# Kernel optimization log

Measured on AMD Instinct MI355X. Metric: run time of the kernel, lower is better.

The kernel has to match this reference:

```python
import jax, jax.numpy as jnp
import numpy as np

N_NODES = 100000
N_EDGES = 1600000
NODE_DIM = 128
EDGE_DIM = 32
HIDDEN = 64
OUT = 64


def setup_inputs() -> dict:
    key = jax.random.key(0)
    ks = jax.random.split(key, 16)
    s = lambda d: 1.0 / np.sqrt(d)
    inp = {
        'node_features': jax.random.normal(ks[0], (N_NODES, NODE_DIM), dtype=jnp.float32),
        'edge_indices': jax.random.randint(ks[1], (2, N_EDGES), 0, N_NODES, dtype=jnp.int64),
        'edge_features': jax.random.normal(ks[2], (N_EDGES, EDGE_DIM), dtype=jnp.float32),
        # node_transform / edge_transform
        'wn': jax.random.uniform(ks[3], (NODE_DIM, HIDDEN), jnp.float32, -s(NODE_DIM), s(NODE_DIM)),
        'bn': jax.random.uniform(ks[4], (HIDDEN,), jnp.float32, -s(NODE_DIM), s(NODE_DIM)),
        'we': jax.random.uniform(ks[5], (EDGE_DIM, HIDDEN), jnp.float32, -s(EDGE_DIM), s(EDGE_DIM)),
        'be': jax.random.uniform(ks[6], (HIDDEN,), jnp.float32, -s(EDGE_DIM), s(EDGE_DIM)),
        # message_mlp: Linear(2H,H) -> ReLU -> Linear(H,OUT)
        'wm1': jax.random.uniform(ks[7], (2 * HIDDEN, HIDDEN), jnp.float32, -s(2 * HIDDEN), s(2 * HIDDEN)),
        'bm1': jax.random.uniform(ks[8], (HIDDEN,), jnp.float32, -s(2 * HIDDEN), s(2 * HIDDEN)),
        'wm2': jax.random.uniform(ks[9], (HIDDEN, OUT), jnp.float32, -s(HIDDEN), s(HIDDEN)),
        'bm2': jax.random.uniform(ks[10], (OUT,), jnp.float32, -s(HIDDEN), s(HIDDEN)),
        # update_mlp: Linear(NODE_DIM+OUT,H) -> ReLU -> Linear(H,OUT)
        'wu1': jax.random.uniform(ks[11], (NODE_DIM + OUT, HIDDEN), jnp.float32, -s(NODE_DIM + OUT), s(NODE_DIM + OUT)),
        'bu1': jax.random.uniform(ks[12], (HIDDEN,), jnp.float32, -s(NODE_DIM + OUT), s(NODE_DIM + OUT)),
        'wu2': jax.random.uniform(ks[13], (HIDDEN, OUT), jnp.float32, -s(HIDDEN), s(HIDDEN)),
        'bu2': jax.random.uniform(ks[14], (OUT,), jnp.float32, -s(HIDDEN), s(HIDDEN)),
    }
    return inp


def reference(node_features, edge_indices, edge_features, wn, bn, we, be,
              wm1, bm1, wm2, bm2, wu1, bu1, wu2, bu2):
    node_emb = node_features @ wn + bn              # [N, H]
    edge_emb = edge_features @ we + be              # [E, H]
    src, dst = edge_indices[0], edge_indices[1]
    messages = jnp.concatenate([node_emb[src], edge_emb], axis=-1)  # [E, 2H]
    messages = jax.nn.relu(messages @ wm1 + bm1) @ wm2 + bm2        # [E, OUT]
    aggregated = jax.ops.segment_sum(messages, dst, num_segments=node_emb.shape[0])  # [N, OUT]
    updated = jnp.concatenate([node_features, aggregated], axis=-1)  # [N, NODE_DIM+OUT]
    return jax.nn.relu(updated @ wu1 + bu1) @ wu2 + bu2              # [N, OUT]
```

## Files before the change

### kernel.cpp

```cpp
#include <hip/hip_runtime.h>

#define NN 100000
#define NE 1600000

typedef __attribute__((ext_vector_type(8))) short bf16x8;
typedef __attribute__((ext_vector_type(4))) float f32x4;

#define OFF_M    0
#define OFF_B    (OFF_M + 16384)
#define OFF_C    (OFF_B + 2048)
#define OFF_W2U  (OFF_C + 64)
#define OFF_D2   (OFF_W2U + 4096)
#define OFF_BFRG (OFF_D2 + 64)
#define OFF_MFRG (OFF_BFRG + 1024)
#define OFF_W2UF (OFF_MFRG + 8192)
#define OFF_WU2F (OFF_W2UF + 2048)
#define OFF_BSUM (OFF_WU2F + 2048)
#define OFF_BOFF (OFF_BSUM + 128)
#define OFF_PRA  (OFF_BOFF + 128)
#define OFF_PRAH (OFF_PRA + NN * 64)
#define OFF_PRU  (OFF_PRAH + NN * 32)
#define OFF_H    (OFF_PRU + NN * 64)
#define OFF_HIST (OFF_H + NN * 64)
#define OFF_CUR  (OFF_HIST + NN)
#define OFF_STRT (OFF_CUR + NN)
#define OFF_HS   (OFF_STRT + NN + 4)
#define WS_UNITS (OFF_HS + NE * 32)

__device__ __forceinline__ unsigned bfr(float x) {
  unsigned u = __float_as_uint(x);
  return (u + 0x7fffu + ((u >> 16) & 1u)) >> 16;
}
__device__ __forceinline__ float bf2f(unsigned short h) {
  return __uint_as_float(((unsigned)h) << 16);
}
__device__ __forceinline__ unsigned addrelu1(unsigned qa, unsigned pb) {
  float lo = __uint_as_float((qa & 0xffffu) << 16) +
             __uint_as_float((pb & 0xffffu) << 16);
  float hi = __uint_as_float(qa & 0xffff0000u) +
             __uint_as_float(pb & 0xffff0000u);
  lo = fmaxf(lo, 0.f);
  hi = fmaxf(hi, 0.f);
  return bfr(lo) | (bfr(hi) << 16);
}
__device__ __forceinline__ uint4 addrelu4(uint4 q, uint4 p) {
  return make_uint4(addrelu1(q.x, p.x), addrelu1(q.y, p.y),
                    addrelu1(q.z, p.z), addrelu1(q.w, p.w));
}

__global__ __launch_bounds__(256) void k_fold(
    const float* __restrict__ wn, const float* __restrict__ bn,
    const float* __restrict__ we, const float* __restrict__ be,
    const float* __restrict__ wm1, const float* __restrict__ bm1,
    const float* __restrict__ wm2, const float* __restrict__ bm2,
    const float* __restrict__ wu1, const float* __restrict__ wu2,
    float* __restrict__ M, float* __restrict__ B, float* __restrict__ c,
    float* __restrict__ W2U, float* __restrict__ d2,
    uint4* __restrict__ Bfrag, uint4* __restrict__ Mfrag,
    uint4* __restrict__ W2Uf, uint4* __restrict__ wu2f) {
  int t = blockIdx.x * 256 + threadIdx.x;
  if (t < 16384) {
    int k = t >> 7, j = t & 127;
    float acc;
    if (j < 64) {
      acc = 0.f;
      for (int h = 0; h < 64; ++h) acc += wn[k * 64 + h] * wm1[h * 64 + j];
    } else {
      acc = wu1[k * 64 + (j - 64)];
    }
    M[t] = acc;
  } else if (t < 16384 + 2048) {
    int u = t - 16384;
    int k = u >> 6, j = u & 63;
    float acc = 0.f;
    for (int h = 0; h < 64; ++h) acc += we[k * 64 + h] * wm1[(64 + h) * 64 + j];
    B[u] = acc;
  } else if (t < 16384 + 2048 + 64) {
    int j = t - (16384 + 2048);
    float acc = bm1[j];
    for (int h = 0; h < 64; ++h)
      acc += bn[h] * wm1[h * 64 + j] + be[h] * wm1[(64 + h) * 64 + j];
    c[j] = acc;
  } else if (t < 16384 + 2048 + 64 + 4096) {
    int u = t - (16384 + 2048 + 64);
    int k = u >> 6, j = u & 63;
    float acc = 0.f;
    for (int h = 0; h < 64; ++h) acc += wm2[k * 64 + h] * wu1[(128 + h) * 64 + j];
    W2U[u] = acc;
  } else if (t < 16384 + 2048 + 64 + 4096 + 64) {
    int j = t - (16384 + 2048 + 64 + 4096);
    float acc = 0.f;
    for (int h = 0; h < 64; ++h) acc += bm2[h] * wu1[(128 + h) * 64 + j];
    d2[j] = acc;
  } else if (t < 16384 + 2048 + 64 + 4096 + 64 + 256) {
    int u = t - (16384 + 2048 + 64 + 4096 + 64);
    int jb = u >> 6, l = u & 63;
    int g = l >> 4, n = l & 15;
    unsigned s[8];
#pragma unroll
    for (int i = 0; i < 8; ++i) {
      int k = g * 8 + i;
      int j = jb * 16 + n;
      float acc = 0.f;
      for (int h = 0; h < 64; ++h)
        acc += we[k * 64 + h] * wm1[(64 + h) * 64 + j];
      s[i] = bfr(acc);
    }
    Bfrag[jb * 64 + l] = make_uint4(s[0] | (s[1] << 16), s[2] | (s[3] << 16),
                                    s[4] | (s[5] << 16), s[6] | (s[7] << 16));
  } else if (t < 16384 + 2048 + 64 + 4096 + 64 + 256 + 2048) {
    int u = t - (16384 + 2048 + 64 + 4096 + 64 + 256);
    int jb = u >> 8, kb = (u >> 6) & 3, l = u & 63;
    int g = l >> 4, n = l & 15;
    int j = jb * 16 + n;
    unsigned s[8];
#pragma unroll
    for (int i = 0; i < 8; ++i) {
      int k = kb * 32 + g * 8 + i;
      float acc;
      if (j < 64) {
        acc = 0.f;
        for (int h = 0; h < 64; ++h) acc += wn[k * 64 + h] * wm1[h * 64 + j];
      } else {
        acc = wu1[k * 64 + (j - 64)];
      }
      s[i] = bfr(acc);
    }
    Mfrag[(jb * 4 + kb) * 64 + l] =
        make_uint4(s[0] | (s[1] << 16), s[2] | (s[3] << 16),
                   s[4] | (s[5] << 16), s[6] | (s[7] << 16));
  } else if (t < 16384 + 2048 + 64 + 4096 + 64 + 256 + 2048 + 512) {
    int u = t - (16384 + 2048 + 64 + 4096 + 64 + 256 + 2048);
    int jk = u >> 6, l = u & 63;
    int jb = jk >> 1, kb = jk & 1;
    int g = l >> 4, n = l & 15;
    int j = jb * 16 + n;
    unsigned s[8];
#pragma unroll
    for (int i = 0; i < 8; ++i) {
      int k = kb * 32 + g * 8 + i;
      float acc = 0.f;
      for (int h = 0; h < 64; ++h)
        acc += wm2[k * 64 + h] * wu1[(128 + h) * 64 + j];
      s[i] = bfr(acc);
    }
    W2Uf[jk * 64 + l] = make_uint4(s[0] | (s[1] << 16), s[2] | (s[3] << 16),
                                   s[4] | (s[5] << 16), s[6] | (s[7] << 16));
  } else if (t < 16384 + 2048 + 64 + 4096 + 64 + 256 + 2048 + 512 + 512) {
    int u = t - (16384 + 2048 + 64 + 4096 + 64 + 256 + 2048 + 512);
    int jk = u >> 6, l = u & 63;
    int jb = jk >> 1, kb = jk & 1;
    int g = l >> 4, n = l & 15;
    unsigned s[8];
#pragma unroll
    for (int i = 0; i < 8; ++i)
      s[i] = bfr(wu2[(size_t)(kb * 32 + g * 8 + i) * 64 + jb * 16 + n]);
    wu2f[jk * 64 + l] = make_uint4(s[0] | (s[1] << 16), s[2] | (s[3] << 16),
                                   s[4] | (s[5] << 16), s[6] | (s[7] << 16));
  }
}

__global__ __launch_bounds__(256) void k_node2(
    const float* __restrict__ nf, const uint4* __restrict__ Mfrag,
    float* __restrict__ PRA, float* __restrict__ PRU) {
  int wib = threadIdx.x >> 6;
  int lane = threadIdx.x & 63;
  int tile = blockIdx.x * 4 + wib;
  if (tile >= NN / 16) return;
  int m = lane & 15, g = lane >> 4;
  int node = tile * 16 + m;

  bf16x8 a[4];
#pragma unroll
  for (int kb = 0; kb < 4; ++kb) {
    const float* __restrict__ rp = &nf[(size_t)node * 128 + kb * 32 + g * 8];
    float4 f0 = *(const float4*)rp;
    float4 f1 = *(const float4*)(rp + 4);
    bf16x8 v;
    v[0] = (short)bfr(f0.x); v[1] = (short)bfr(f0.y);
    v[2] = (short)bfr(f0.z); v[3] = (short)bfr(f0.w);
    v[4] = (short)bfr(f1.x); v[5] = (short)bfr(f1.y);
    v[6] = (short)bfr(f1.z); v[7] = (short)bfr(f1.w);
    a[kb] = v;
  }

  const bf16x8* __restrict__ mfp = (const bf16x8*)Mfrag;
#pragma unroll
  for (int jb = 0; jb < 8; ++jb) {
    f32x4 acc = {0.f, 0.f, 0.f, 0.f};
    acc = __builtin_amdgcn_mfma_f32_16x16x32_bf16(a[0], mfp[(jb * 4 + 0) * 64 + lane], acc, 0, 0, 0);
    acc = __builtin_amdgcn_mfma_f32_16x16x32_bf16(a[1], mfp[(jb * 4 + 1) * 64 + lane], acc, 0, 0, 0);
    acc = __builtin_amdgcn_mfma_f32_16x16x32_bf16(a[2], mfp[(jb * 4 + 2) * 64 + lane], acc, 0, 0, 0);
    acc = __builtin_amdgcn_mfma_f32_16x16x32_bf16(a[3], mfp[(jb * 4 + 3) * 64 + lane], acc, 0, 0, 0);
    float* __restrict__ dst = (jb < 4) ? PRA : PRU;
    int col = (jb & 3) * 16 + m;
#pragma unroll
    for (int r = 0; r < 4; ++r) {
      int row = tile * 16 + g * 4 + r;
      dst[(size_t)row * 64 + col] = acc[r];
    }
  }
}

__global__ __launch_bounds__(256) void k_prah(
    const float2* __restrict__ PRA2, unsigned* __restrict__ PRAh) {
  int t = blockIdx.x * 256 + threadIdx.x;
  if (t < NN * 32) {
    float2 v = PRA2[t];
    PRAh[t] = bfr(v.x) | (bfr(v.y) << 16);
  }
}

__global__ __launch_bounds__(256) void k_hist(const int* __restrict__ idx,
                                              int* __restrict__ hist) {
  int e = blockIdx.x * 256 + threadIdx.x;
  if (e < NE) atomicAdd(&hist[idx[NE + e]], 1);
}

__global__ __launch_bounds__(1024) void k_scanA(const int* __restrict__ hist,
                                                int* __restrict__ strt,
                                                int* __restrict__ bsum) {
  __shared__ int lds[1024];
  int t = threadIdx.x;
  int i = blockIdx.x * 1024 + t;
  int v = (i < NN) ? hist[i] : 0;
  lds[t] = v;
  __syncthreads();
  for (int off = 1; off < 1024; off <<= 1) {
    int u = (t >= off) ? lds[t - off] : 0;
    __syncthreads();
    lds[t] += u;
    __syncthreads();
  }
  if (i < NN) strt[i] = lds[t] - v;
  if (t == 1023) bsum[blockIdx.x] = lds[1023];
}

__global__ __launch_bounds__(128) void k_scanB(const int* __restrict__ bsum,
                                               int* __restrict__ boff,
                                               int* __restrict__ strt,
                                               int nblocks) {
  __shared__ int lds[128];
  int t = threadIdx.x;
  int v = (t < nblocks) ? bsum[t] : 0;
  lds[t] = v;
  __syncthreads();
  for (int off = 1; off < 128; off <<= 1) {
    int u = (t >= off) ? lds[t - off] : 0;
    __syncthreads();
    lds[t] += u;
    __syncthreads();
  }
  if (t < nblocks) boff[t] = lds[t] - v;
  if (t == 127) strt[NN] = lds[127];
}

__global__ __launch_bounds__(1024) void k_scanC(int* __restrict__ strt,
                                                const int* __restrict__ boff) {
  int i = blockIdx.x * 1024 + threadIdx.x;
  if (i < NN) strt[i] += boff[blockIdx.x];
}

__global__ __launch_bounds__(256) void k_msgh(
    const int* __restrict__ idx, const int* __restrict__ strt,
    int* __restrict__ cursor, const float* __restrict__ ef,
    const uint4* __restrict__ Bfrag, const float* __restrict__ c,
    const uint4* __restrict__ PRAh, unsigned short* __restrict__ hS) {
  __shared__ unsigned short ldsQ[4][16 * 72];
  __shared__ int slotA[4][16];
  __shared__ int srcA[4][16];
  int wib = threadIdx.x >> 6;
  int lane = threadIdx.x & 63;
  int m = lane & 15, g = lane >> 4;
  int tile = blockIdx.x * 4 + wib;

  if (lane < 16) {
    int e = tile * 16 + m;
    int src = idx[e];
    int dst = idx[NE + e];
    int pos = atomicAdd(&cursor[dst], 1);
    slotA[wib][m] = strt[dst] + pos;
    srcA[wib][m] = src;
  }

  const float* __restrict__ rp = &ef[(size_t)(tile * 16 + m) * 32 + g * 8];
  float4 f0 = *(const float4*)rp;
  float4 f1 = *(const float4*)(rp + 4);
  bf16x8 a;
  a[0] = (short)bfr(f0.x); a[1] = (short)bfr(f0.y);
  a[2] = (short)bfr(f0.z); a[3] = (short)bfr(f0.w);
  a[4] = (short)bfr(f1.x); a[5] = (short)bfr(f1.y);
  a[6] = (short)bfr(f1.z); a[7] = (short)bfr(f1.w);

  const bf16x8* __restrict__ bfp = (const bf16x8*)Bfrag;
  bf16x8 b0 = bfp[0 * 64 + lane];
  bf16x8 b1 = bfp[1 * 64 + lane];
  bf16x8 b2 = bfp[2 * 64 + lane];
  bf16x8 b3 = bfp[3 * 64 + lane];
  float cl0 = c[0 * 16 + m], cl1 = c[1 * 16 + m];
  float cl2 = c[2 * 16 + m], cl3 = c[3 * 16 + m];

  f32x4 z = {0.f, 0.f, 0.f, 0.f};
  f32x4 q0 = __builtin_amdgcn_mfma_f32_16x16x32_bf16(a, b0, z, 0, 0, 0);
  f32x4 q1 = __builtin_amdgcn_mfma_f32_16x16x32_bf16(a, b1, z, 0, 0, 0);
  f32x4 q2 = __builtin_amdgcn_mfma_f32_16x16x32_bf16(a, b2, z, 0, 0, 0);
  f32x4 q3 = __builtin_amdgcn_mfma_f32_16x16x32_bf16(a, b3, z, 0, 0, 0);

  unsigned short* __restrict__ lq = &ldsQ[wib][0];
#pragma unroll
  for (int r = 0; r < 4; ++r) {
    int mp = g * 4 + r;
    lq[mp * 72 + 0 * 16 + m] = (unsigned short)bfr(q0[r] + cl0);
    lq[mp * 72 + 1 * 16 + m] = (unsigned short)bfr(q1[r] + cl1);
    lq[mp * 72 + 2 * 16 + m] = (unsigned short)bfr(q2[r] + cl2);
    lq[mp * 72 + 3 * 16 + m] = (unsigned short)bfr(q3[r] + cl3);
  }
  __syncthreads();

  int m2 = lane >> 2, lo = lane & 3;
  uint4 w0 = *(const uint4*)&ldsQ[wib][m2 * 72 + lo * 16];
  uint4 w1 = *(const uint4*)&ldsQ[wib][m2 * 72 + lo * 16 + 8];
  int slot = slotA[wib][m2];
  int src = srcA[wib][m2];
  uint4 p0 = PRAh[(size_t)src * 8 + lo * 2];
  uint4 p1 = PRAh[(size_t)src * 8 + lo * 2 + 1];
  uint4 h0 = addrelu4(w0, p0);
  uint4 h1 = addrelu4(w1, p1);
  uint4* __restrict__ qp = (uint4*)(hS + (size_t)slot * 64);
  qp[lo * 2] = h0;
  qp[lo * 2 + 1] = h1;
}

__global__ __launch_bounds__(256) void k_sum(
    const unsigned short* __restrict__ hS, const int* __restrict__ strt,
    float* __restrict__ H) {
  int wib = threadIdx.x >> 6;
  int lane = threadIdx.x & 63;
  int n = blockIdx.x * 4 + wib;
  if (n >= NN) return;
  int s0 = strt[n], s1 = strt[n + 1];
  float acc = 0.f;
  int s = s0;
  for (; s + 4 <= s1; s += 4) {
    unsigned short a0 = hS[(size_t)(s + 0) * 64 + lane];
    unsigned short a1 = hS[(size_t)(s + 1) * 64 + lane];
    unsigned short a2 = hS[(size_t)(s + 2) * 64 + lane];
    unsigned short a3 = hS[(size_t)(s + 3) * 64 + lane];
    acc += (bf2f(a0) + bf2f(a1)) + (bf2f(a2) + bf2f(a3));
  }
  for (; s < s1; ++s) acc += bf2f(hS[(size_t)s * 64 + lane]);
  H[(size_t)n * 64 + lane] = acc;
}

__global__ __launch_bounds__(256) void k_update5(
    const float* __restrict__ H, const int* __restrict__ strt,
    const float* __restrict__ PRU,
    const uint4* __restrict__ W2Uf, const float* __restrict__ d2,
    const float* __restrict__ bu1,
    const uint4* __restrict__ wu2f, const float* __restrict__ bu2,
    float* __restrict__ out) {
  __shared__ unsigned short ldsH[4][16 * 72];
  int wib = threadIdx.x >> 6;
  int lane = threadIdx.x & 63;
  int tile = blockIdx.x * 4 + wib;
  if (tile >= NN / 16) return;
  int m = lane & 15, g = lane >> 4;
  int node = tile * 16 + m;

  bf16x8 ah[2];
#pragma unroll
  for (int kb = 0; kb < 2; ++kb) {
    const float* __restrict__ rp = &H[(size_t)node * 64 + kb * 32 + g * 8];
    float4 f0 = *(const float4*)rp;
    float4 f1 = *(const float4*)(rp + 4);
    bf16x8 v;
    v[0] = (short)bfr(f0.x); v[1] = (short)bfr(f0.y);
    v[2] = (short)bfr(f0.z); v[3] = (short)bfr(f0.w);
    v[4] = (short)bfr(f1.x); v[5] = (short)bfr(f1.y);
    v[6] = (short)bfr(f1.z); v[7] = (short)bfr(f1.w);
    ah[kb] = v;
  }

  const bf16x8* __restrict__ w2p = (const bf16x8*)W2Uf;
  const bf16x8* __restrict__ wup = (const bf16x8*)wu2f;
  unsigned short* __restrict__ lh = &ldsH[wib][0];

#pragma unroll
  for (int jb = 0; jb < 4; ++jb) {
    f32x4 acc = {0.f, 0.f, 0.f, 0.f};
    acc = __builtin_amdgcn_mfma_f32_16x16x32_bf16(ah[0], w2p[(jb * 2 + 0) * 64 + lane], acc, 0, 0, 0);
    acc = __builtin_amdgcn_mfma_f32_16x16x32_bf16(ah[1], w2p[(jb * 2 + 1) * 64 + lane], acc, 0, 0, 0);
    int col = jb * 16 + m;
    float dc = d2[col], bc = bu1[col];
#pragma unroll
    for (int r = 0; r < 4; ++r) {
      int row = tile * 16 + g * 4 + r;
      float deg = (float)(strt[row + 1] - strt[row]);
      float pre = acc[r] + PRU[(size_t)row * 64 + col] + deg * dc + bc;
      lh[(g * 4 + r) * 72 + col] = (unsigned short)bfr(fmaxf(pre, 0.f));
    }
  }
  __syncthreads();

  bf16x8 a2[2];
  a2[0] = *(const bf16x8*)&lh[m * 72 + 0 * 32 + g * 8];
  a2[1] = *(const bf16x8*)&lh[m * 72 + 1 * 32 + g * 8];
#pragma unroll
  for (int jb = 0; jb < 4; ++jb) {
    f32x4 acc = {0.f, 0.f, 0.f, 0.f};
    acc = __builtin_amdgcn_mfma_f32_16x16x32_bf16(a2[0], wup[(jb * 2 + 0) * 64 + lane], acc, 0, 0, 0);
    acc = __builtin_amdgcn_mfma_f32_16x16x32_bf16(a2[1], wup[(jb * 2 + 1) * 64 + lane], acc, 0, 0, 0);
    int col = jb * 16 + m;
    float bc = bu2[col];
#pragma unroll
    for (int r = 0; r < 4; ++r) {
      int row = tile * 16 + g * 4 + r;
      out[(size_t)row * 64 + col] = acc[r] + bc;
    }
  }
}

__global__ __launch_bounds__(256) void k_edge_at(
    const int* __restrict__ idx, const float* __restrict__ ef,
    const float* __restrict__ B, const float* __restrict__ c,
    const float* __restrict__ wm2, const float* __restrict__ bm2,
    const float* __restrict__ PRA, float* __restrict__ agg) {
  int e = blockIdx.x * 256 + threadIdx.x;
  if (e >= NE) return;
  int src = idx[e];
  int dst = idx[NE + e];
  float efr[32];
#pragma unroll
  for (int k = 0; k < 32; k += 4)
    *(float4*)&efr[k] = *(const float4*)&ef[(size_t)e * 32 + k];
  float m[64];
#pragma unroll
  for (int o = 0; o < 64; ++o) m[o] = bm2[o];
  const float* __restrict__ prs = &PRA[(size_t)src * 64];
#pragma unroll 1
  for (int jc = 0; jc < 64; jc += 16) {
    float q[16];
#pragma unroll
    for (int jj = 0; jj < 16; ++jj) q[jj] = c[jc + jj];
#pragma unroll
    for (int k = 0; k < 32; ++k) {
      float ev = efr[k];
#pragma unroll
      for (int jj = 0; jj < 16; ++jj) q[jj] += ev * B[k * 64 + jc + jj];
    }
#pragma unroll
    for (int jj = 0; jj < 16; ++jj) {
      float h = fmaxf(prs[jc + jj] + q[jj], 0.f);
#pragma unroll
      for (int o = 0; o < 64; ++o) m[o] += h * wm2[(jc + jj) * 64 + o];
    }
  }
  float* __restrict__ ap = &agg[(size_t)dst * 64];
#pragma unroll
  for (int o = 0; o < 64; ++o) atomicAdd(&ap[o], m[o]);
}

__global__ __launch_bounds__(256) void k_update_at(
    const float* __restrict__ agg, const float* __restrict__ PRU,
    const float* __restrict__ wu1, const float* __restrict__ bu1,
    const float* __restrict__ wu2, const float* __restrict__ bu2,
    float* __restrict__ out) {
  int n = blockIdx.x * 256 + threadIdx.x;
  if (n >= NN) return;
  float ar[64];
#pragma unroll
  for (int k = 0; k < 64; k += 4)
    *(float4*)&ar[k] = *(const float4*)&agg[(size_t)n * 64 + k];
  float acc[64];
#pragma unroll
  for (int o = 0; o < 64; ++o) acc[o] = bu2[o];
  const float* __restrict__ prs = &PRU[(size_t)n * 64];
#pragma unroll 1
  for (int jc = 0; jc < 64; jc += 16) {
    float q[16];
#pragma unroll
    for (int jj = 0; jj < 16; ++jj) q[jj] = bu1[jc + jj];
#pragma unroll
    for (int k = 0; k < 64; ++k) {
      float av = ar[k];
#pragma unroll
      for (int jj = 0; jj < 16; ++jj) q[jj] += av * wu1[(128 + k) * 64 + jc + jj];
    }
#pragma unroll
    for (int jj = 0; jj < 16; ++jj) {
      float h = fmaxf(prs[jc + jj] + q[jj], 0.f);
#pragma unroll
      for (int o = 0; o < 64; ++o) acc[o] += h * wu2[(jc + jj) * 64 + o];
    }
  }
#pragma unroll
  for (int o = 0; o < 64; o += 4)
    *(float4*)&out[(size_t)n * 64 + o] = make_float4(acc[o], acc[o + 1], acc[o + 2], acc[o + 3]);
}

extern "C" void kernel_launch(void* const* d_in, const int* in_sizes, int n_in,
                              void* d_out, int out_size, void* d_ws, size_t ws_size,
                              hipStream_t stream) {
  const float* nf  = (const float*)d_in[0];
  const int*   idx = (const int*)d_in[1];
  const float* ef  = (const float*)d_in[2];
  const float* wn  = (const float*)d_in[3];
  const float* bn  = (const float*)d_in[4];
  const float* we  = (const float*)d_in[5];
  const float* be  = (const float*)d_in[6];
  const float* wm1 = (const float*)d_in[7];
  const float* bm1 = (const float*)d_in[8];
  const float* wm2 = (const float*)d_in[9];
  const float* bm2 = (const float*)d_in[10];
  const float* wu1 = (const float*)d_in[11];
  const float* bu1 = (const float*)d_in[12];
  const float* wu2 = (const float*)d_in[13];
  const float* bu2 = (const float*)d_in[14];
  float* out = (float*)d_out;

  float* ws   = (float*)d_ws;
  float* M    = ws + OFF_M;
  float* B    = ws + OFF_B;
  float* c    = ws + OFF_C;
  float* W2U  = ws + OFF_W2U;
  float* d2   = ws + OFF_D2;
  uint4* Bfrg = (uint4*)(ws + OFF_BFRG);
  uint4* Mfrg = (uint4*)(ws + OFF_MFRG);
  uint4* W2Uf = (uint4*)(ws + OFF_W2UF);
  uint4* wu2f = (uint4*)(ws + OFF_WU2F);
  int*   bsum = (int*)(ws + OFF_BSUM);
  int*   boff = (int*)(ws + OFF_BOFF);
  float* PRA  = ws + OFF_PRA;
  unsigned* PRAh = (unsigned*)(ws + OFF_PRAH);
  float* PRU  = ws + OFF_PRU;
  float* H    = ws + OFF_H;
  int*   hist = (int*)(ws + OFF_HIST);
  int*   cur  = (int*)(ws + OFF_CUR);
  int*   strt = (int*)(ws + OFF_STRT);
  unsigned short* hS = (unsigned short*)(ws + OFF_HS);

  const int SCAN_BLOCKS = (NN + 1023) / 1024;
  const int FOLD_THREADS = 16384 + 2048 + 64 + 4096 + 64 + 256 + 2048 + 512 + 512;
  const int NTILE = NN / 16;

  k_fold<<<(FOLD_THREADS + 255) / 256, 256, 0, stream>>>(
      wn, bn, we, be, wm1, bm1, wm2, bm2, wu1, wu2,
      M, B, c, W2U, d2, Bfrg, Mfrg, W2Uf, wu2f);
  k_node2<<<(NTILE + 3) / 4, 256, 0, stream>>>(nf, Mfrg, PRA, PRU);
  k_prah<<<(NN * 32 + 255) / 256, 256, 0, stream>>>((const float2*)PRA, PRAh);

  if (ws_size >= (size_t)WS_UNITS * 4) {
    hipMemsetAsync(hist, 0, (size_t)2 * NN * sizeof(int), stream);
    k_hist<<<(NE + 255) / 256, 256, 0, stream>>>(idx, hist);
    k_scanA<<<SCAN_BLOCKS, 1024, 0, stream>>>(hist, strt, bsum);
    k_scanB<<<1, 128, 0, stream>>>(bsum, boff, strt, SCAN_BLOCKS);
    k_scanC<<<SCAN_BLOCKS, 1024, 0, stream>>>(strt, boff);
    k_msgh<<<NE / 16 / 4, 256, 0, stream>>>(idx, strt, cur, ef, Bfrg, c,
                                            (const uint4*)PRAh, hS);
    k_sum<<<(NN + 3) / 4, 256, 0, stream>>>(hS, strt, H);
    k_update5<<<(NTILE + 3) / 4, 256, 0, stream>>>(
        H, strt, PRU, W2Uf, d2, bu1, wu2f, bu2, out);
  } else {
    hipMemsetAsync(H, 0, (size_t)NN * 64 * sizeof(float), stream);
    k_edge_at<<<(NE + 255) / 256, 256, 0, stream>>>(idx, ef, B, c, wm2, bm2, PRA, H);
    k_update_at<<<(NN + 255) / 256, 256, 0, stream>>>(
        H, PRU, wu1, bu1, wu2, bu2, out);
  }
}
```

Before: 370.0 us.

## Fuse bf16 PRA packing into node kernel, prefetch gather, store H as bf16

The separate k_prah conversion kernel is removed: k_node2 now stages the bf16 PRA tile in LDS and writes packed PRAh directly, and skips the fp32 PRA store on the fast path. k_msgh issues the src-indexed PRAh gather at kernel start, so its latency overlaps the edge MFMA work instead of following the barrier. k_sum writes the aggregated H as packed bf16, which halves that buffer's traffic, and k_update5 loads it directly as MFMA operands and hoists the degree loads. Together these cut one launch and several fp32 round-trips through global memory. H now carries bf16 precision, but it was already rounded to bf16 before the MFMA, so accuracy should be essentially unchanged.

Measured after the change: 361.8 us. -2.2%, faster.

```diff
diff --git a/kernel.cpp b/kernel.cpp
--- a/kernel.cpp
+++ b/kernel.cpp
@@ -162,7 +162,9 @@
 
 __global__ __launch_bounds__(256) void k_node2(
     const float* __restrict__ nf, const uint4* __restrict__ Mfrag,
-    float* __restrict__ PRA, float* __restrict__ PRU) {
+    float* __restrict__ PRA, uint4* __restrict__ PRAh,
+    float* __restrict__ PRU, int writePRA) {
+  __shared__ unsigned short ldsP[4][16 * 72];
   int wib = threadIdx.x >> 6;
   int lane = threadIdx.x & 63;
   int tile = blockIdx.x * 4 + wib;
@@ -185,6 +187,7 @@
   }
 
   const bf16x8* __restrict__ mfp = (const bf16x8*)Mfrag;
+  unsigned short* __restrict__ lp = &ldsP[wib][0];
 #pragma unroll
   for (int jb = 0; jb < 8; ++jb) {
     f32x4 acc = {0.f, 0.f, 0.f, 0.f};
@@ -192,23 +195,30 @@
     acc = __builtin_amdgcn_mfma_f32_16x16x32_bf16(a[1], mfp[(jb * 4 + 1) * 64 + lane], acc, 0, 0, 0);
     acc = __builtin_amdgcn_mfma_f32_16x16x32_bf16(a[2], mfp[(jb * 4 + 2) * 64 + lane], acc, 0, 0, 0);
     acc = __builtin_amdgcn_mfma_f32_16x16x32_bf16(a[3], mfp[(jb * 4 + 3) * 64 + lane], acc, 0, 0, 0);
-    float* __restrict__ dst = (jb < 4) ? PRA : PRU;
     int col = (jb & 3) * 16 + m;
-#pragma unroll
-    for (int r = 0; r < 4; ++r) {
-      int row = tile * 16 + g * 4 + r;
-      dst[(size_t)row * 64 + col] = acc[r];
-    }
-  }
-}
-
-__global__ __launch_bounds__(256) void k_prah(
-    const float2* __restrict__ PRA2, unsigned* __restrict__ PRAh) {
-  int t = blockIdx.x * 256 + threadIdx.x;
-  if (t < NN * 32) {
-    float2 v = PRA2[t];
-    PRAh[t] = bfr(v.x) | (bfr(v.y) << 16);
-  }
+    if (jb < 4) {
+#pragma unroll
+      for (int r = 0; r < 4; ++r)
+        lp[(g * 4 + r) * 72 + col] = (unsigned short)bfr(acc[r]);
+      if (writePRA) {
+#pragma unroll
+        for (int r = 0; r < 4; ++r)
+          PRA[(size_t)(tile * 16 + g * 4 + r) * 64 + col] = acc[r];
+      }
+    } else {
+#pragma unroll
+      for (int r = 0; r < 4; ++r)
+        PRU[(size_t)(tile * 16 + g * 4 + r) * 64 + col] = acc[r];
+    }
+  }
+  __syncthreads();
+
+  int m2 = lane >> 2, lo = lane & 3;
+  uint4 w0 = *(const uint4*)&ldsP[wib][m2 * 72 + lo * 16];
+  uint4 w1 = *(const uint4*)&ldsP[wib][m2 * 72 + lo * 16 + 8];
+  uint4* __restrict__ pp = &PRAh[(size_t)(tile * 16 + m2) * 8];
+  pp[lo * 2] = w0;
+  pp[lo * 2 + 1] = w1;
 }
 
 __global__ __launch_bounds__(256) void k_hist(const int* __restrict__ idx,
@@ -268,19 +278,21 @@
     const uint4* __restrict__ PRAh, unsigned short* __restrict__ hS) {
   __shared__ unsigned short ldsQ[4][16 * 72];
   __shared__ int slotA[4][16];
-  __shared__ int srcA[4][16];
   int wib = threadIdx.x >> 6;
   int lane = threadIdx.x & 63;
   int m = lane & 15, g = lane >> 4;
   int tile = blockIdx.x * 4 + wib;
 
+  int m2 = lane >> 2, lo = lane & 3;
+  int src6 = idx[tile * 16 + m2];
+  uint4 p0 = PRAh[(size_t)src6 * 8 + lo * 2];
+  uint4 p1 = PRAh[(size_t)src6 * 8 + lo * 2 + 1];
+
   if (lane < 16) {
     int e = tile * 16 + m;
-    int src = idx[e];
     int dst = idx[NE + e];
     int pos = atomicAdd(&cursor[dst], 1);
     slotA[wib][m] = strt[dst] + pos;
-    srcA[wib][m] = src;
   }
 
   const float* __restrict__ rp = &ef[(size_t)(tile * 16 + m) * 32 + g * 8];
@@ -317,13 +329,9 @@
   }
   __syncthreads();
 
-  int m2 = lane >> 2, lo = lane & 3;
   uint4 w0 = *(const uint4*)&ldsQ[wib][m2 * 72 + lo * 16];
   uint4 w1 = *(const uint4*)&ldsQ[wib][m2 * 72 + lo * 16 + 8];
   int slot = slotA[wib][m2];
-  int src = srcA[wib][m2];
-  uint4 p0 = PRAh[(size_t)src * 8 + lo * 2];
-  uint4 p1 = PRAh[(size_t)src * 8 + lo * 2 + 1];
   uint4 h0 = addrelu4(w0, p0);
   uint4 h1 = addrelu4(w1, p1);
   uint4* __restrict__ qp = (uint4*)(hS + (size_t)slot * 64);
@@ -333,7 +341,7 @@
 
 __global__ __launch_bounds__(256) void k_sum(
     const unsigned short* __restrict__ hS, const int* __restrict__ strt,
-    float* __restrict__ H) {
+    unsigned* __restrict__ Hb) {
   int wib = threadIdx.x >> 6;
   int lane = threadIdx.x & 63;
   int n = blockIdx.x * 4 + wib;
@@ -349,11 +357,13 @@
     acc += (bf2f(a0) + bf2f(a1)) + (bf2f(a2) + bf2f(a3));
   }
   for (; s < s1; ++s) acc += bf2f(hS[(size_t)s * 64 + lane]);
-  H[(size_t)n * 64 + lane] = acc;
+  float other = __shfl_xor(acc, 1);
+  if ((lane & 1) == 0)
+    Hb[(size_t)n * 32 + (lane >> 1)] = bfr(acc) | (bfr(other) << 16);
 }
 
 __global__ __launch_bounds__(256) void k_update5(
-    const float* __restrict__ H, const int* __restrict__ strt,
+    const unsigned* __restrict__ Hb, const int* __restrict__ strt,
     const float* __restrict__ PRU,
     const uint4* __restrict__ W2Uf, const float* __restrict__ d2,
     const float* __restrict__ bu1,
@@ -368,17 +378,14 @@
   int node = tile * 16 + m;
 
   bf16x8 ah[2];
-#pragma unroll
-  for (int kb = 0; kb < 2; ++kb) {
-    const float* __restrict__ rp = &H[(size_t)node * 64 + kb * 32 + g * 8];
-    float4 f0 = *(const float4*)rp;
-    float4 f1 = *(const float4*)(rp + 4);
-    bf16x8 v;
-    v[0] = (short)bfr(f0.x); v[1] = (short)bfr(f0.y);
-    v[2] = (short)bfr(f0.z); v[3] = (short)bfr(f0.w);
-    v[4] = (short)bfr(f1.x); v[5] = (short)bfr(f1.y);
-    v[6] = (short)bfr(f1.z); v[7] = (short)bfr(f1.w);
-    ah[kb] = v;
+  ah[0] = *(const bf16x8*)&Hb[(size_t)node * 32 + 0 * 16 + g * 4];
+  ah[1] = *(const bf16x8*)&Hb[(size_t)node * 32 + 1 * 16 + g * 4];
+
+  float deg[4];
+#pragma unroll
+  for (int r = 0; r < 4; ++r) {
+    int row = tile * 16 + g * 4 + r;
+    deg[r] = (float)(strt[row + 1] - strt[row]);
   }
 
   const bf16x8* __restrict__ w2p = (const bf16x8*)W2Uf;
@@ -395,8 +402,7 @@
 #pragma unroll
     for (int r = 0; r < 4; ++r) {
       int row = tile * 16 + g * 4 + r;
-      float deg = (float)(strt[row + 1] - strt[row]);
-      float pre = acc[r] + PRU[(size_t)row * 64 + col] + deg * dc + bc;
+      float pre = acc[r] + PRU[(size_t)row * 64 + col] + deg[r] * dc + bc;
       lh[(g * 4 + r) * 72 + col] = (unsigned short)bfr(fmaxf(pre, 0.f));
     }
   }
@@ -531,9 +537,10 @@
   int*   bsum = (int*)(ws + OFF_BSUM);
   int*   boff = (int*)(ws + OFF_BOFF);
   float* PRA  = ws + OFF_PRA;
-  unsigned* PRAh = (unsigned*)(ws + OFF_PRAH);
+  uint4* PRAh = (uint4*)(ws + OFF_PRAH);
   float* PRU  = ws + OFF_PRU;
   float* H    = ws + OFF_H;
+  unsigned* Hb = (unsigned*)(ws + OFF_H);
   int*   hist = (int*)(ws + OFF_HIST);
   int*   cur  = (int*)(ws + OFF_CUR);
   int*   strt = (int*)(ws + OFF_STRT);
@@ -543,23 +550,25 @@
   const int FOLD_THREADS = 16384 + 2048 + 64 + 4096 + 64 + 256 + 2048 + 512 + 512;
   const int NTILE = NN / 16;
 
+  int fast = (ws_size >= (size_t)WS_UNITS * 4);
+
   k_fold<<<(FOLD_THREADS + 255) / 256, 256, 0, stream>>>(
       wn, bn, we, be, wm1, bm1, wm2, bm2, wu1, wu2,
       M, B, c, W2U, d2, Bfrg, Mfrg, W2Uf, wu2f);
-  k_node2<<<(NTILE + 3) / 4, 256, 0, stream>>>(nf, Mfrg, PRA, PRU);
-  k_prah<<<(NN * 32 + 255) / 256, 256, 0, stream>>>((const float2*)PRA, PRAh);
-
-  if (ws_size >= (size_t)WS_UNITS * 4) {
+  k_node2<<<(NTILE + 3) / 4, 256, 0, stream>>>(nf, Mfrg, PRA, PRAh, PRU,
+                                               fast ? 0 : 1);
+
+  if (fast) {
     hipMemsetAsync(hist, 0, (size_t)2 * NN * sizeof(int), stream);
     k_hist<<<(NE + 255) / 256, 256, 0, stream>>>(idx, hist);
     k_scanA<<<SCAN_BLOCKS, 1024, 0, stream>>>(hist, strt, bsum);
     k_scanB<<<1, 128, 0, stream>>>(bsum, boff, strt, SCAN_BLOCKS);
     k_scanC<<<SCAN_BLOCKS, 1024, 0, stream>>>(strt, boff);
     k_msgh<<<NE / 16 / 4, 256, 0, stream>>>(idx, strt, cur, ef, Bfrg, c,
-                                            (const uint4*)PRAh, hS);
-    k_sum<<<(NN + 3) / 4, 256, 0, stream>>>(hS, strt, H);
+                                            PRAh, hS);
+    k_sum<<<(NN + 3) / 4, 256, 0, stream>>>(hS, strt, Hb);
     k_update5<<<(NTILE + 3) / 4, 256, 0, stream>>>(
-        H, strt, PRU, W2Uf, d2, bu1, wu2f, bu2, out);
+        Hb, strt, PRU, W2Uf, d2, bu1, wu2f, bu2, out);
   } else {
     hipMemsetAsync(H, 0, (size_t)NN * 64 * sizeof(float), stream);
     k_edge_at<<<(NE + 255) / 256, 256, 0, stream>>>(idx, ef, B, c, wm2, bm2, PRA, H);
```
